# Kernel tuning notes

Measured on AMD Instinct MI355X. Metric: run time of the kernel, lower is better.

Reference implementation:

```python
import jax, jax.numpy as jnp
import numpy as np

N_NODES = 384
HEIGHT = 60
LN_EPS = 1e-5


def setup_inputs() -> dict:
    key = jax.random.key(0)
    ks = jax.random.split(key, 6)
    C = 256
    E = 3072
    x = jax.random.normal(ks[0], (N_NODES, C, HEIGHT), dtype=jnp.float32)
    edge_attr = jax.random.normal(ks[1], (E, 5), dtype=jnp.float32)
    edge_index = jax.random.randint(ks[2], (2, E), 0, N_NODES)
    W_edge = jax.random.normal(ks[3], (5, C), dtype=jnp.float32) * 0.3
    b_edge = jnp.zeros((C,), dtype=jnp.float32)
    W_conv = jax.random.normal(ks[4], (C, 3 * C), dtype=jnp.float32) * (1.0 / np.sqrt(3 * C))
    ln_gamma = jnp.ones((C, HEIGHT), dtype=jnp.float32)
    ln_beta = jnp.zeros((C, HEIGHT), dtype=jnp.float32)
    return {"x": x, "edge_attr": edge_attr, "edge_index": edge_index,
            "W_edge": W_edge, "b_edge": b_edge, "W_conv": W_conv,
            "ln_gamma": ln_gamma, "ln_beta": ln_beta}


def reference(x, edge_attr, edge_index, W_edge, b_edge, W_conv, ln_gamma, ln_beta):
    # x: (N, C, 60); PyG convention: edge_index[0]=source (j), edge_index[1]=target (i)
    C = x.shape[1]
    src, dst = edge_index[0], edge_index[1]
    h_i = x[dst]                    # (E, C, 60) gather target features
    h_j = x[src]                    # (E, C, 60) gather source features
    ea = edge_attr @ W_edge + b_edge            # (E, C) edge Linear
    ea = jnp.broadcast_to(ea[:, :, None], h_i.shape)  # repeat over height
    h = jnp.concatenate([h_i, h_j - h_i, ea], axis=1)  # (E, 3C, 60)
    # Conv1d kernel_size=1, bias=False -> channel contraction
    m = jnp.einsum('ech,oc->eoh', h, W_conv)    # (E, C, 60)
    # LayerNorm over (C, 60) per edge
    mu = jnp.mean(m, axis=(1, 2), keepdims=True)
    var = jnp.var(m, axis=(1, 2), keepdims=True)
    m = (m - mu) * jax.lax.rsqrt(var + LN_EPS) * ln_gamma + ln_beta
    m = jax.nn.relu(m)
    # aggr='add' scatter into target nodes
    out = jax.ops.segment_sum(m.reshape(m.shape[0], C * HEIGHT), dst,
                              num_segments=N_NODES)
    return out.reshape(N_NODES, C, HEIGHT)
```

## Files before the change

### kernel.cpp

```cpp
#include <hip/hip_runtime.h>

#define N_NODES 384
#define CCH 256
#define HT 60
#define CH (CCH*HT)
#define CH4 (CH/4)
#define LN_EPS 1e-5f

typedef __attribute__((ext_vector_type(8))) short bf16x8;
typedef __attribute__((ext_vector_type(4))) float f32x4;

__device__ inline unsigned short f2bf(float f) {
    unsigned int u = __float_as_uint(f);
    unsigned int r = (u + 0x7FFF + ((u >> 16) & 1)) >> 16;
    return (unsigned short)r;
}
__device__ inline float bf2f(unsigned short u) {
    return __uint_as_float(((unsigned int)u) << 16);
}

__global__ __launch_bounds__(1024) void k_setup(const float* __restrict__ Wc,
                                                unsigned short* __restrict__ Wfrag) {
    int idx = blockIdx.x * 1024 + threadIdx.x;
    int j = idx & 7, lane = (idx >> 3) & 63, ks = (idx >> 9) & 7, mt = idx >> 12;
    int o = mt * 16 + (lane & 15);
    int c = ks * 32 + (lane >> 4) * 8 + j;
    float v;
    if (o < 256) v = Wc[o * 768 + c] - Wc[o * 768 + 256 + c];
    else         v = Wc[(o - 256) * 768 + 256 + c];
    Wfrag[idx] = f2bf(v);
}

__global__ __launch_bounds__(256) void k_node_mfma(const float* __restrict__ x,
                                                   const unsigned short* __restrict__ Wfrag,
                                                   unsigned short* __restrict__ Abf,
                                                   unsigned short* __restrict__ Bbf) {
    __shared__ unsigned short xT[32 * 256];
    int n = blockIdx.x, half = blockIdx.y, tid = threadIdx.x;

    const float4* xg = (const float4*)(x + (size_t)n * CH);
    if (half == 0) {
        for (int i = tid; i < 2048; i += 256) {
            int c = i >> 3, jj = i & 7;
            int r0 = jj * 4;
            float4 v = xg[c * 15 + jj];
            xT[(r0+0) * 256 + (c ^ (((r0+0) & 7) << 3))] = f2bf(v.x);
            xT[(r0+1) * 256 + (c ^ (((r0+1) & 7) << 3))] = f2bf(v.y);
            xT[(r0+2) * 256 + (c ^ (((r0+2) & 7) << 3))] = f2bf(v.z);
            xT[(r0+3) * 256 + (c ^ (((r0+3) & 7) << 3))] = f2bf(v.w);
        }
    } else {
        for (int i = tid; i < 4 * 256; i += 256) {
            int r = 28 + (i >> 8), c = i & 255;
            xT[r * 256 + (c ^ ((r & 7) << 3))] = 0;
        }
        for (int i = tid; i < 1792; i += 256) {
            int c = i / 7, jj = i - c * 7;
            int r0 = jj * 4;
            float4 v = xg[c * 15 + 8 + jj];
            xT[(r0+0) * 256 + (c ^ (((r0+0) & 7) << 3))] = f2bf(v.x);
            xT[(r0+1) * 256 + (c ^ (((r0+1) & 7) << 3))] = f2bf(v.y);
            xT[(r0+2) * 256 + (c ^ (((r0+2) & 7) << 3))] = f2bf(v.z);
            xT[(r0+3) * 256 + (c ^ (((r0+3) & 7) << 3))] = f2bf(v.w);
        }
    }
    __syncthreads();

    int w = tid >> 6, lane = tid & 63;
    int l15 = lane & 15, lg = lane >> 4;

    f32x4 acc[8][2];
#pragma unroll
    for (int mt = 0; mt < 8; ++mt)
#pragma unroll
        for (int nt = 0; nt < 2; ++nt)
            acc[mt][nt] = (f32x4){0.f, 0.f, 0.f, 0.f};

    const unsigned short* wbase = Wfrag + ((size_t)(w * 8) * 8) * 64 * 8;
    for (int ks = 0; ks < 8; ++ks) {
        bf16x8 bfr[2];
#pragma unroll
        for (int nt = 0; nt < 2; ++nt) {
            int row = nt * 16 + l15;
            int col = ks * 32 + lg * 8;
            int idx = row * 256 + (col ^ ((row & 7) << 3));
            bfr[nt] = *(const bf16x8*)(&xT[idx]);
        }
#pragma unroll
        for (int mt = 0; mt < 8; ++mt) {
            const bf16x8 afr = *(const bf16x8*)(wbase + (((size_t)mt * 8 + ks) * 64 + lane) * 8);
#pragma unroll
            for (int nt = 0; nt < 2; ++nt)
                acc[mt][nt] = __builtin_amdgcn_mfma_f32_16x16x32_bf16(afr, bfr[nt], acc[mt][nt], 0, 0, 0);
        }
    }

#pragma unroll
    for (int mt = 0; mt < 8; ++mt) {
        int mtg = w * 8 + mt;
        int obase = mtg * 16 + 4 * lg;
        unsigned short* dst0 = (obase < 256)
            ? (Abf + (size_t)n * CH + (size_t)obase * 60)
            : (Bbf + (size_t)n * CH + (size_t)(obase - 256) * 60);
#pragma unroll
        for (int nt = 0; nt < 2; ++nt) {
            int h = half * 32 + nt * 16 + l15;
            if (h < 60) {
#pragma unroll
                for (int r = 0; r < 4; ++r)
                    dst0[r * 60 + h] = f2bf(acc[mt][nt][r]);
            }
        }
    }
}

__global__ __launch_bounds__(256) void k_prepscal(const unsigned short* __restrict__ Abf,
                                                  const unsigned short* __restrict__ Bbf,
                                                  const float* __restrict__ Wc,
                                                  const float* __restrict__ We,
                                                  const float* __restrict__ be,
                                                  const int* __restrict__ dst, int E,
                                                  float* __restrict__ RAB,
                                                  float4* __restrict__ Sc,
                                                  float* __restrict__ M,
                                                  float* __restrict__ bias0,
                                                  int* __restrict__ offs,
                                                  int* __restrict__ elist) {
    int b = blockIdx.x;
    int tid = threadIdx.x, w = tid >> 6, lane = tid & 63;
    if (b == 0) {
        __shared__ int cnt[N_NODES];
        __shared__ int sc0[N_NODES], sc1[N_NODES];
        for (int i = tid; i < N_NODES; i += 256) cnt[i] = 0;
        __syncthreads();
        for (int e = tid; e < E; e += 256) atomicAdd(&cnt[dst[e]], 1);
        __syncthreads();
        for (int i = tid; i < N_NODES; i += 256) sc0[i] = cnt[i];
        __syncthreads();
        int flip = 0;
        for (int d = 1; d < N_NODES; d <<= 1) {
            const int* s_ = flip ? sc1 : sc0;
            int* d_ = flip ? sc0 : sc1;
            for (int i = tid; i < N_NODES; i += 256)
                d_[i] = s_[i] + (i >= d ? s_[i - d] : 0);
            __syncthreads();
            flip ^= 1;
        }
        const int* pos = flip ? sc1 : sc0;
        for (int i = tid; i < N_NODES; i += 256) {
            offs[i + 1] = pos[i];
            cnt[i] = (i == 0) ? 0 : pos[i - 1];
        }
        if (tid == 0) offs[0] = 0;
        __syncthreads();
        for (int e = tid; e < E; e += 256) {
            int d = dst[e];
            elist[atomicAdd(&cnt[d], 1)] = e;
        }
        __syncthreads();
        for (int n2 = tid; n2 < N_NODES; n2 += 256) {
            int lo = (n2 == 0) ? 0 : pos[n2 - 1], hi = pos[n2];
            for (int i = lo + 1; i < hi; ++i) {
                int key = elist[i]; int j = i - 1;
                while (j >= lo && elist[j] > key) { elist[j + 1] = elist[j]; --j; }
                elist[j + 1] = key;
            }
        }
        return;
    }
    if (b == 1) {
        int o = tid;
        float m0=0,m1=0,m2=0,m3=0,m4=0,bb=0;
        for (int k = 0; k < 256; ++k) {
            float w3 = Wc[o * 768 + 512 + k];
            m0 += We[0*256+k] * w3;
            m1 += We[1*256+k] * w3;
            m2 += We[2*256+k] * w3;
            m3 += We[3*256+k] * w3;
            m4 += We[4*256+k] * w3;
            bb += be[k] * w3;
        }
        M[0*256+o]=m0; M[1*256+o]=m1; M[2*256+o]=m2; M[3*256+o]=m3; M[4*256+o]=m4;
        bias0[o] = bb;
        return;
    }
    {
        __shared__ float red[16];
        int n = b - 2;
        const ushort4* Ab = (const ushort4*)(Abf + (size_t)n * CH + tid * 60);
        const ushort4* Bb = (const ushort4*)(Bbf + (size_t)n * CH + tid * 60);
        float rsA = 0.f, qA = 0.f, rsB = 0.f, qB = 0.f;
#pragma unroll
        for (int i = 0; i < 15; ++i) {
            ushort4 a = Ab[i], bb2 = Bb[i];
#pragma unroll
            for (int j = 0; j < 4; ++j) {
                float va = bf2f(((const unsigned short*)&a)[j]);
                float vb = bf2f(((const unsigned short*)&bb2)[j]);
                rsA += va; qA += va * va;
                rsB += vb; qB += vb * vb;
            }
        }
        RAB[(size_t)n * 512 + tid] = rsA;
        RAB[(size_t)n * 512 + 256 + tid] = rsB;
        float sA = rsA, sB = rsB;
#pragma unroll
        for (int o = 32; o >= 1; o >>= 1) {
            sA += __shfl_xor(sA, o, 64); qA += __shfl_xor(qA, o, 64);
            sB += __shfl_xor(sB, o, 64); qB += __shfl_xor(qB, o, 64);
        }
        if (lane == 0) { red[w*4]=sA; red[w*4+1]=qA; red[w*4+2]=sB; red[w*4+3]=qB; }
        __syncthreads();
        if (tid == 0) {
            Sc[n] = make_float4(red[0]+red[4]+red[8]+red[12],
                                red[1]+red[5]+red[9]+red[13],
                                red[2]+red[6]+red[10]+red[14],
                                red[3]+red[7]+red[11]+red[15]);
        }
    }
}

__global__ __launch_bounds__(256) void k_estats(const unsigned short* __restrict__ Abf,
                                                const unsigned short* __restrict__ Bbf,
                                                const float* __restrict__ ea,
                                                const float* __restrict__ M,
                                                const float* __restrict__ bias0,
                                                const int* __restrict__ srcA,
                                                const int* __restrict__ dstA,
                                                const float* __restrict__ RAB,
                                                const float4* __restrict__ Sc,
                                                float* __restrict__ cbuf,
                                                float2* __restrict__ stats) {
    __shared__ float red[16];
    int e = blockIdx.x;
    int tid = threadIdx.x, w = tid >> 6, lane = tid & 63;
    int s = srcA[e], d = dstA[e];

    float ev0 = ea[e*5], ev1 = ea[e*5+1], ev2 = ea[e*5+2], ev3 = ea[e*5+3], ev4 = ea[e*5+4];
    int o = tid;
    float c = bias0[o] + ev0*M[o] + ev1*M[256+o] + ev2*M[512+o] + ev3*M[768+o] + ev4*M[1024+o];
    cbuf[(size_t)e * 256 + o] = c;
    float sc = c, sc2 = c * c;
    float dots = (RAB[(size_t)d * 512 + o] + RAB[(size_t)s * 512 + 256 + o]) * c;

    const ushort4* Ab = (const ushort4*)(Abf + (size_t)d * CH);
    const ushort4* Bb = (const ushort4*)(Bbf + (size_t)s * CH);
    float dot = 0.f;
#pragma unroll
    for (int r = 0; r < 15; ++r) {
        ushort4 a = Ab[tid + 256 * r];
        ushort4 b = Bb[tid + 256 * r];
        dot += bf2f(a.x) * bf2f(b.x) + bf2f(a.y) * bf2f(b.y)
             + bf2f(a.z) * bf2f(b.z) + bf2f(a.w) * bf2f(b.w);
    }

#pragma unroll
    for (int o2 = 32; o2 >= 1; o2 >>= 1) {
        sc   += __shfl_xor(sc, o2, 64);
        sc2  += __shfl_xor(sc2, o2, 64);
        dots += __shfl_xor(dots, o2, 64);
        dot  += __shfl_xor(dot, o2, 64);
    }
    if (lane == 0) { red[w*4]=sc; red[w*4+1]=sc2; red[w*4+2]=dots; red[w*4+3]=dot; }
    __syncthreads();
    if (tid == 0) {
        float S_c   = red[0] + red[4] + red[8]  + red[12];
        float S_c2  = red[1] + red[5] + red[9]  + red[13];
        float S_dts = red[2] + red[6] + red[10] + red[14];
        float S_dot = red[3] + red[7] + red[11] + red[15];
        float4 scd = Sc[d], scs = Sc[s];
        float S1 = scd.x + scs.z + 60.f * S_c;
        float S2 = scd.y + scs.w + 60.f * S_c2 + 2.f * (S_dot + S_dts);
        float mu = S1 * (1.0f / (float)CH);
        float var = S2 * (1.0f / (float)CH) - mu * mu;
        stats[e] = make_float2(mu, rsqrtf(var + LN_EPS));
    }
}

__global__ __launch_bounds__(256) void k_apply(const unsigned short* __restrict__ Abf,
                                               const unsigned short* __restrict__ Bbf,
                                               const float* __restrict__ cbuf,
                                               const float2* __restrict__ stats,
                                               const int* __restrict__ srcArr,
                                               const int* __restrict__ offsets,
                                               const int* __restrict__ elist,
                                               const float* __restrict__ gamma,
                                               const float* __restrict__ beta,
                                               float* __restrict__ out) {
    int b = blockIdx.x;
    int cg8 = b & 7;
    int n = b >> 3;
    int tid = threadIdx.x;
    size_t sbase = (size_t)n * CH + (size_t)cg8 * 1920;
    const ushort4* Ab = (const ushort4*)(Abf + sbase);
    const float4*  g4 = (const float4*)(gamma + (size_t)cg8 * 1920);
    const float4*  b4 = (const float4*)(beta  + (size_t)cg8 * 1920);
    bool act1 = (tid < 224);

    float4 af[2], gv[2], bv[2], acc[2];
    int ci[2];
#pragma unroll
    for (int r = 0; r < 2; ++r) {
        acc[r] = make_float4(0.f, 0.f, 0.f, 0.f);
        af[r] = make_float4(0.f, 0.f, 0.f, 0.f);
        gv[r] = make_float4(0.f, 0.f, 0.f, 0.f);
        bv[r] = make_float4(0.f, 0.f, 0.f, 0.f);
        ci[r] = 0;
    }
#pragma unroll
    for (int r = 0; r < 2; ++r) {
        if (r == 0 || act1) {
            int i = tid + 256 * r;
            ci[r] = i / 15;
            ushort4 aw = Ab[i];
            af[r].x = bf2f(aw.x); af[r].y = bf2f(aw.y);
            af[r].z = bf2f(aw.z); af[r].w = bf2f(aw.w);
            gv[r] = g4[i];
            bv[r] = b4[i];
        }
    }

    int lo = offsets[n], hi = offsets[n + 1];
    int k = lo;
    for (; k + 1 < hi; k += 2) {
        int e0 = elist[k], e1 = elist[k + 1];
        int s0 = srcArr[e0], s1 = srcArr[e1];
        float2 st0 = stats[e0], st1 = stats[e1];
        const ushort4* B0 = (const ushort4*)(Bbf + (size_t)s0 * CH + (size_t)cg8 * 1920);
        const ushort4* B1 = (const ushort4*)(Bbf + (size_t)s1 * CH + (size_t)cg8 * 1920);
        const float* c0 = cbuf + (size_t)e0 * 256 + cg8 * 32;
        const float* c1 = cbuf + (size_t)e1 * 256 + cg8 * 32;
#pragma unroll
        for (int r = 0; r < 2; ++r) {
            if (r == 0 || act1) {
                int i = tid + 256 * r;
                ushort4 bw0 = B0[i];
                ushort4 bw1 = B1[i];
                float cc0 = c0[ci[r]];
                float cc1 = c1[ci[r]];
                float m0x = af[r].x + bf2f(bw0.x) + cc0;
                float m0y = af[r].y + bf2f(bw0.y) + cc0;
                float m0z = af[r].z + bf2f(bw0.z) + cc0;
                float m0w = af[r].w + bf2f(bw0.w) + cc0;
                float m1x = af[r].x + bf2f(bw1.x) + cc1;
                float m1y = af[r].y + bf2f(bw1.y) + cc1;
                float m1z = af[r].z + bf2f(bw1.z) + cc1;
                float m1w = af[r].w + bf2f(bw1.w) + cc1;
                acc[r].x += fmaxf((m0x - st0.x) * st0.y * gv[r].x + bv[r].x, 0.f);
                acc[r].y += fmaxf((m0y - st0.x) * st0.y * gv[r].y + bv[r].y, 0.f);
                acc[r].z += fmaxf((m0z - st0.x) * st0.y * gv[r].z + bv[r].z, 0.f);
                acc[r].w += fmaxf((m0w - st0.x) * st0.y * gv[r].w + bv[r].w, 0.f);
                acc[r].x += fmaxf((m1x - st1.x) * st1.y * gv[r].x + bv[r].x, 0.f);
                acc[r].y += fmaxf((m1y - st1.x) * st1.y * gv[r].y + bv[r].y, 0.f);
                acc[r].z += fmaxf((m1z - st1.x) * st1.y * gv[r].z + bv[r].z, 0.f);
                acc[r].w += fmaxf((m1w - st1.x) * st1.y * gv[r].w + bv[r].w, 0.f);
            }
        }
    }
    if (k < hi) {
        int e = elist[k];
        int s = srcArr[e];
        float2 st = stats[e];
        const ushort4* Bb = (const ushort4*)(Bbf + (size_t)s * CH + (size_t)cg8 * 1920);
        const float* cc = cbuf + (size_t)e * 256 + cg8 * 32;
#pragma unroll
        for (int r = 0; r < 2; ++r) {
            if (r == 0 || act1) {
                int i = tid + 256 * r;
                float ccv = cc[ci[r]];
                ushort4 bw = Bb[i];
                float mx = af[r].x + bf2f(bw.x) + ccv;
                float my = af[r].y + bf2f(bw.y) + ccv;
                float mz = af[r].z + bf2f(bw.z) + ccv;
                float mw = af[r].w + bf2f(bw.w) + ccv;
                acc[r].x += fmaxf((mx - st.x) * st.y * gv[r].x + bv[r].x, 0.f);
                acc[r].y += fmaxf((my - st.x) * st.y * gv[r].y + bv[r].y, 0.f);
                acc[r].z += fmaxf((mz - st.x) * st.y * gv[r].z + bv[r].z, 0.f);
                acc[r].w += fmaxf((mw - st.x) * st.y * gv[r].w + bv[r].w, 0.f);
            }
        }
    }
    float4* ob = (float4*)(out + sbase);
#pragma unroll
    for (int r = 0; r < 2; ++r)
        if (r == 0 || act1) ob[tid + 256 * r] = acc[r];
}

extern "C" void kernel_launch(void* const* d_in, const int* in_sizes, int n_in,
                              void* d_out, int out_size, void* d_ws, size_t ws_size,
                              hipStream_t stream) {
    const float* x     = (const float*)d_in[0];
    const float* ea    = (const float*)d_in[1];
    const int*   ei    = (const int*)d_in[2];
    const float* We    = (const float*)d_in[3];
    const float* be    = (const float*)d_in[4];
    const float* Wc    = (const float*)d_in[5];
    const float* gamma = (const float*)d_in[6];
    const float* beta  = (const float*)d_in[7];
    const int E = in_sizes[2] / 2;
    const int* src = ei;
    const int* dst = ei + E;

    char* ws = (char*)d_ws;
    size_t off = 0;
    auto alloc = [&](size_t bytes) -> void* {
        void* p = ws + off;
        off += (bytes + 255) & ~(size_t)255;
        return p;
    };
    unsigned short* Abf    = (unsigned short*)alloc((size_t)N_NODES * CH * 2);
    unsigned short* Bbf    = (unsigned short*)alloc((size_t)N_NODES * CH * 2);
    float*          cbuf   = (float*)alloc((size_t)E * 256 * 4);
    float2*         stats  = (float2*)alloc((size_t)E * 8);
    unsigned short* Wfrag  = (unsigned short*)alloc(512 * 256 * 2);
    float*          M      = (float*)alloc(5 * 256 * 4);
    float*          bias0  = (float*)alloc(256 * 4);
    float*          RAB    = (float*)alloc((size_t)N_NODES * 512 * 4);
    float4*         Sc     = (float4*)alloc((size_t)N_NODES * 16);
    int*            offs   = (int*)alloc((N_NODES + 1) * 4);
    int*            elist  = (int*)alloc((size_t)E * 4);

    k_setup<<<128, 1024, 0, stream>>>(Wc, Wfrag);
    k_node_mfma<<<dim3(N_NODES, 2), 256, 0, stream>>>(x, Wfrag, Abf, Bbf);
    k_prepscal<<<2 + N_NODES, 256, 0, stream>>>(Abf, Bbf, Wc, We, be, dst, E,
                                                RAB, Sc, M, bias0, offs, elist);
    k_estats<<<E, 256, 0, stream>>>(Abf, Bbf, ea, M, bias0, src, dst, RAB, Sc,
                                    cbuf, stats);
    k_apply<<<N_NODES * 8, 256, 0, stream>>>(Abf, Bbf, cbuf, stats, src, offs, elist,
                                             gamma, beta, (float*)d_out);
}
```

Measured before the change: 99.43 us.

## Move per-edge A·B dot products into prep kernel and shrink stats kernel

The heavy per-edge dot product between the bf16 A (dst) and B (src) node features is split into eight channel-group chunks, one wavefront each. These chunks run as extra blocks in the prep kernel, so they execute alongside the node reductions, and write partial sums to a new buffer. The stats kernel becomes one wavefront per edge that computes the edge-attribute term and combines the eight partials, which removes the block-level shared-memory reduction. This spreads the bandwidth-bound dot work over more parallel waves and saves one large launch's worth of work, at the cost of an extra small buffer and a kernel that mixes several jobs.

Result: faster. 85.06 us (-14.5%).

```diff
diff --git a/kernel.cpp b/kernel.cpp
--- a/kernel.cpp
+++ b/kernel.cpp
@@ -114,18 +114,20 @@
     }
 }
 
-__global__ __launch_bounds__(256) void k_prepscal(const unsigned short* __restrict__ Abf,
+__global__ __launch_bounds__(256) void k_prepdots(const unsigned short* __restrict__ Abf,
                                                   const unsigned short* __restrict__ Bbf,
                                                   const float* __restrict__ Wc,
                                                   const float* __restrict__ We,
                                                   const float* __restrict__ be,
-                                                  const int* __restrict__ dst, int E,
+                                                  const int* __restrict__ srcA,
+                                                  const int* __restrict__ dstA, int E,
                                                   float* __restrict__ RAB,
                                                   float4* __restrict__ Sc,
                                                   float* __restrict__ M,
                                                   float* __restrict__ bias0,
                                                   int* __restrict__ offs,
-                                                  int* __restrict__ elist) {
+                                                  int* __restrict__ elist,
+                                                  float* __restrict__ Gp8) {
     int b = blockIdx.x;
     int tid = threadIdx.x, w = tid >> 6, lane = tid & 63;
     if (b == 0) {
@@ -133,7 +135,7 @@
         __shared__ int sc0[N_NODES], sc1[N_NODES];
         for (int i = tid; i < N_NODES; i += 256) cnt[i] = 0;
         __syncthreads();
-        for (int e = tid; e < E; e += 256) atomicAdd(&cnt[dst[e]], 1);
+        for (int e = tid; e < E; e += 256) atomicAdd(&cnt[dstA[e]], 1);
         __syncthreads();
         for (int i = tid; i < N_NODES; i += 256) sc0[i] = cnt[i];
         __syncthreads();
@@ -154,7 +156,7 @@
         if (tid == 0) offs[0] = 0;
         __syncthreads();
         for (int e = tid; e < E; e += 256) {
-            int d = dst[e];
+            int d = dstA[e];
             elist[atomicAdd(&cnt[d], 1)] = e;
         }
         __syncthreads();
@@ -184,7 +186,7 @@
         bias0[o] = bb;
         return;
     }
-    {
+    if (b < 2 + N_NODES) {
         __shared__ float red[16];
         int n = b - 2;
         const ushort4* Ab = (const ushort4*)(Abf + (size_t)n * CH + tid * 60);
@@ -217,60 +219,74 @@
                                 red[2]+red[6]+red[10]+red[14],
                                 red[3]+red[7]+red[11]+red[15]);
         }
-    }
-}
-
-__global__ __launch_bounds__(256) void k_estats(const unsigned short* __restrict__ Abf,
-                                                const unsigned short* __restrict__ Bbf,
-                                                const float* __restrict__ ea,
+        return;
+    }
+    {
+        int g = b - (2 + N_NODES);
+        int cg8 = g & 7;
+        int ew = g >> 3;
+        int e = ew * 4 + w;
+        if (e >= E) return;
+        int s = srcA[e], d = dstA[e];
+        const ushort4* Ab = (const ushort4*)(Abf + (size_t)d * CH + (size_t)cg8 * 1920);
+        const ushort4* Bb = (const ushort4*)(Bbf + (size_t)s * CH + (size_t)cg8 * 1920);
+        float dot = 0.f;
+#pragma unroll
+        for (int r = 0; r < 7; ++r) {
+            int i = lane + 64 * r;
+            ushort4 a = Ab[i], bb2 = Bb[i];
+            dot += bf2f(a.x) * bf2f(bb2.x) + bf2f(a.y) * bf2f(bb2.y)
+                 + bf2f(a.z) * bf2f(bb2.z) + bf2f(a.w) * bf2f(bb2.w);
+        }
+        if (lane < 32) {
+            int i = lane + 448;
+            ushort4 a = Ab[i], bb2 = Bb[i];
+            dot += bf2f(a.x) * bf2f(bb2.x) + bf2f(a.y) * bf2f(bb2.y)
+                 + bf2f(a.z) * bf2f(bb2.z) + bf2f(a.w) * bf2f(bb2.w);
+        }
+#pragma unroll
+        for (int o2 = 32; o2 >= 1; o2 >>= 1)
+            dot += __shfl_xor(dot, o2, 64);
+        if (lane == 0) Gp8[(size_t)e * 8 + cg8] = dot;
+    }
+}
+
+__global__ __launch_bounds__(256) void k_stats2(const float* __restrict__ ea,
                                                 const float* __restrict__ M,
                                                 const float* __restrict__ bias0,
                                                 const int* __restrict__ srcA,
-                                                const int* __restrict__ dstA,
+                                                const int* __restrict__ dstA, int E,
                                                 const float* __restrict__ RAB,
                                                 const float4* __restrict__ Sc,
+                                                const float* __restrict__ Gp8,
                                                 float* __restrict__ cbuf,
                                                 float2* __restrict__ stats) {
-    __shared__ float red[16];
-    int e = blockIdx.x;
-    int tid = threadIdx.x, w = tid >> 6, lane = tid & 63;
+    int w = threadIdx.x >> 6, lane = threadIdx.x & 63;
+    int e = blockIdx.x * 4 + w;
+    if (e >= E) return;
     int s = srcA[e], d = dstA[e];
-
     float ev0 = ea[e*5], ev1 = ea[e*5+1], ev2 = ea[e*5+2], ev3 = ea[e*5+3], ev4 = ea[e*5+4];
-    int o = tid;
-    float c = bias0[o] + ev0*M[o] + ev1*M[256+o] + ev2*M[512+o] + ev3*M[768+o] + ev4*M[1024+o];
-    cbuf[(size_t)e * 256 + o] = c;
-    float sc = c, sc2 = c * c;
-    float dots = (RAB[(size_t)d * 512 + o] + RAB[(size_t)s * 512 + 256 + o]) * c;
-
-    const ushort4* Ab = (const ushort4*)(Abf + (size_t)d * CH);
-    const ushort4* Bb = (const ushort4*)(Bbf + (size_t)s * CH);
-    float dot = 0.f;
-#pragma unroll
-    for (int r = 0; r < 15; ++r) {
-        ushort4 a = Ab[tid + 256 * r];
-        ushort4 b = Bb[tid + 256 * r];
-        dot += bf2f(a.x) * bf2f(b.x) + bf2f(a.y) * bf2f(b.y)
-             + bf2f(a.z) * bf2f(b.z) + bf2f(a.w) * bf2f(b.w);
-    }
-
+    float sc = 0.f, sc2 = 0.f, dots = 0.f;
+#pragma unroll
+    for (int r = 0; r < 4; ++r) {
+        int o = lane + 64 * r;
+        float c = bias0[o] + ev0*M[o] + ev1*M[256+o] + ev2*M[512+o] + ev3*M[768+o] + ev4*M[1024+o];
+        cbuf[(size_t)e * 256 + o] = c;
+        sc += c; sc2 += c * c;
+        dots += (RAB[(size_t)d * 512 + o] + RAB[(size_t)s * 512 + 256 + o]) * c;
+    }
+    float g = (lane < 8) ? Gp8[(size_t)e * 8 + lane] : 0.f;
 #pragma unroll
     for (int o2 = 32; o2 >= 1; o2 >>= 1) {
         sc   += __shfl_xor(sc, o2, 64);
         sc2  += __shfl_xor(sc2, o2, 64);
         dots += __shfl_xor(dots, o2, 64);
-        dot  += __shfl_xor(dot, o2, 64);
-    }
-    if (lane == 0) { red[w*4]=sc; red[w*4+1]=sc2; red[w*4+2]=dots; red[w*4+3]=dot; }
-    __syncthreads();
-    if (tid == 0) {
-        float S_c   = red[0] + red[4] + red[8]  + red[12];
-        float S_c2  = red[1] + red[5] + red[9]  + red[13];
-        float S_dts = red[2] + red[6] + red[10] + red[14];
-        float S_dot = red[3] + red[7] + red[11] + red[15];
+        g    += __shfl_xor(g, o2, 64);
+    }
+    if (lane == 0) {
         float4 scd = Sc[d], scs = Sc[s];
-        float S1 = scd.x + scs.z + 60.f * S_c;
-        float S2 = scd.y + scs.w + 60.f * S_c2 + 2.f * (S_dot + S_dts);
+        float S1 = scd.x + scs.z + 60.f * sc;
+        float S2 = scd.y + scs.w + 60.f * sc2 + 2.f * (g + dots);
         float mu = S1 * (1.0f / (float)CH);
         float var = S2 * (1.0f / (float)CH) - mu * mu;
         stats[e] = make_float2(mu, rsqrtf(var + LN_EPS));
@@ -417,15 +433,17 @@
     float*          bias0  = (float*)alloc(256 * 4);
     float*          RAB    = (float*)alloc((size_t)N_NODES * 512 * 4);
     float4*         Sc     = (float4*)alloc((size_t)N_NODES * 16);
+    float*          Gp8    = (float*)alloc((size_t)E * 8 * 4);
     int*            offs   = (int*)alloc((N_NODES + 1) * 4);
     int*            elist  = (int*)alloc((size_t)E * 4);
 
+    int ndot = ((E + 3) / 4) * 8;
     k_setup<<<128, 1024, 0, stream>>>(Wc, Wfrag);
     k_node_mfma<<<dim3(N_NODES, 2), 256, 0, stream>>>(x, Wfrag, Abf, Bbf);
-    k_prepscal<<<2 + N_NODES, 256, 0, stream>>>(Abf, Bbf, Wc, We, be, dst, E,
-                                                RAB, Sc, M, bias0, offs, elist);
-    k_estats<<<E, 256, 0, stream>>>(Abf, Bbf, ea, M, bias0, src, dst, RAB, Sc,
-                                    cbuf, stats);
+    k_prepdots<<<2 + N_NODES + ndot, 256, 0, stream>>>(Abf, Bbf, Wc, We, be, src, dst, E,
+                                                       RAB, Sc, M, bias0, offs, elist, Gp8);
+    k_stats2<<<(E + 3) / 4, 256, 0, stream>>>(ea, M, bias0, src, dst, E, RAB, Sc, Gp8,
+                                              cbuf, stats);
     k_apply<<<N_NODES * 8, 256, 0, stream>>>(Abf, Bbf, cbuf, stats, src, offs, elist,
                                              gamma, beta, (float*)d_out);
 }
```
